# Performance work log

Hardware: AMD Instinct MI355X
Metric: run time of the kernel (lower is better)

Reference implementation:

```python
import jax, jax.numpy as jnp
import numpy as np
from jax import lax

LMBD = 0.1      # l1 penalty weight (init kwarg lmbd)
TOL = 1e-4      # convergence tolerance (init kwarg tol)
N_ITERS = 1000  # max ISTA iterations
DICT_SIZE = 1024
INPUT_DIM = 512
BATCH = 256


def setup_inputs() -> dict:
    key = jax.random.key(0)
    kx, kd = jax.random.split(key)
    # Dictionary parameter: randn rows normalized to unit l2 norm (as in _init_dict)
    D = jax.random.normal(kd, (DICT_SIZE, INPUT_DIM), dtype=jnp.float32)
    D = D / jnp.linalg.norm(D, axis=1, keepdims=True)
    x = jax.random.normal(kx, (BATCH, INPUT_DIM), dtype=jnp.float32)
    return {"x": x, "D": D}


def reference(x, D):
    # lr = 0.99 / max eigenvalue of Gram(D)  (as in _init_lr, done under no_grad)
    gram = D @ D.T  # [dict, dict]
    lr = 0.99 / jnp.max(jnp.linalg.eigvalsh(gram))
    thresh = lr * LMBD
    h0 = jnp.zeros((x.shape[0], D.shape[0]), dtype=x.dtype)  # [batch, dict]

    def cond(state):
        _, i, delta = state
        return (i < N_ITERS) & (delta >= TOL)

    def body(state):
        h, i, _ = state
        resid = x - h @ D          # [batch, input_dim]
        g = resid @ D.T            # [batch, dict]
        a = h + lr * g
        h_new = jnp.sign(a) * jnp.maximum(jnp.abs(a) - thresh, 0.0)  # soft-threshold
        delta = jnp.max(jnp.linalg.norm(h_new - h, axis=1))
        return (h_new, i + 1, delta)

    h, _, _ = lax.while_loop(cond, body, (h0, jnp.int32(0), jnp.float32(jnp.inf)))
    return h
```

## Files before the change

kernel.cpp:

```cpp
#include <hip/hip_runtime.h>
#include <math.h>

#define DICT 1024
#define IN_DIM 512
#define BATCH 256
#define LMBD_F 0.1f
#define TOL2 1e-8f
#define MAX_ITERS 1000
#define LM 64

#define OFF_G      0u
#define OFF_B      1048576u
#define OFF_HA     1310720u
#define OFF_W      1572864u
#define OFF_RDP    1573888u
#define OFF_FLG    1577984u
#define OFF_PM     1582080u
#define OFF_BF     1582592u
#define OFF_GBF    2106880u

typedef __attribute__((ext_vector_type(8))) short short8v;
typedef __attribute__((ext_vector_type(4))) float f32x4;
typedef __attribute__((ext_vector_type(4))) int i32x4;

#define MFMA16(a, b, c) __builtin_amdgcn_mfma_f32_16x16x32_bf16(a, b, c, 0, 0, 0)

__device__ __forceinline__ ushort f2bf(float v) {
    union { float f; unsigned u; } x; x.f = v;
    unsigned r = x.u + 0x7fffu + ((x.u >> 16) & 1u);
    return (ushort)(r >> 16);
}
__device__ __forceinline__ float bf2f(ushort b) {
    union { unsigned u; float f; } x; x.u = ((unsigned)b) << 16;
    return x.f;
}
__device__ __forceinline__ float softthr(float aa, float th) {
    float s = fabsf(aa) - th;
    return s > 0.f ? copysignf(s, aa) : 0.f;
}

__device__ __forceinline__ void vmdrain() { asm volatile("s_waitcnt vmcnt(0)" ::: "memory"); }
__device__ __forceinline__ unsigned ld_flag(const unsigned* p) {
    unsigned v;
    asm volatile("global_load_dword %0, %1, off sc1\ns_waitcnt vmcnt(0)" : "=v"(v) : "v"(p) : "memory");
    return v;
}
__device__ __forceinline__ void st_flag(unsigned* p, unsigned v) {
    asm volatile("global_store_dword %0, %1, off sc1" :: "v"(p), "v"(v) : "memory");
}
__device__ __forceinline__ float ld_f_sc(const float* p) {
    float v;
    asm volatile("global_load_dword %0, %1, off sc1\ns_waitcnt vmcnt(0)" : "=v"(v) : "v"(p) : "memory");
    return v;
}
__device__ __forceinline__ void st_f_sc(float* p, float v) {
    asm volatile("global_store_dword %0, %1, off sc1" :: "v"(p), "v"(v) : "memory");
}
__device__ __forceinline__ f32x4 ld_f4_sc(const float* p) {
    f32x4 v;
    asm volatile("global_load_dwordx4 %0, %1, off sc1\ns_waitcnt vmcnt(0)" : "=v"(v) : "v"(p) : "memory");
    return v;
}
__device__ __forceinline__ void st_u_sc(unsigned* p, unsigned v) {
    asm volatile("global_store_dword %0, %1, off sc1" :: "v"(p), "v"(v) : "memory");
}
__device__ __forceinline__ void ld_a16(i32x4* d, const void* p) {
    asm volatile("global_load_dwordx4 %0, %1, off sc1" : "=v"(*d) : "v"(p));
}
__device__ __forceinline__ void ld_u_nw(unsigned* d, const unsigned* p) {
    asm volatile("global_load_dword %0, %1, off sc1" : "=v"(*d) : "v"(p));
}
__device__ __forceinline__ void ld_f_nw(float* d, const float* p) {
    asm volatile("global_load_dword %0, %1, off sc1" : "=v"(*d) : "v"(p));
}

__global__ void k_init(float* ws) {
    int t = threadIdx.x;
    unsigned* flg = (unsigned*)(ws + OFF_FLG);
#pragma unroll
    for (int j = 0; j < 4; ++j) flg[t + 1024 * j] = 0u;
#pragma unroll
    for (int j = 0; j < 4; ++j) ws[OFF_RDP + t + 1024 * j] = 1e30f;
    if (t == 0) *(unsigned*)(ws + OFF_PM) = 0u;
}

__global__ void k_gemm_nt(float* __restrict__ C, const float* __restrict__ A,
                          const float* __restrict__ B, int M, int N, int K) {
    __shared__ float As[32][33];
    __shared__ float Bs[32][33];
    const int tid = threadIdx.x;
    const int m0 = blockIdx.y * 32, n0 = blockIdx.x * 32;
    const int lrw = tid >> 3;
    const int lc4 = (tid & 7) * 4;
    const int ty = tid >> 4, tx = tid & 15;
    float acc00 = 0, acc01 = 0, acc10 = 0, acc11 = 0;
    for (int k0 = 0; k0 < K; k0 += 32) {
        float4 av = *(const float4*)&A[(m0 + lrw) * K + k0 + lc4];
        float4 bv = *(const float4*)&B[(n0 + lrw) * K + k0 + lc4];
        __syncthreads();
        As[lrw][lc4 + 0] = av.x; As[lrw][lc4 + 1] = av.y;
        As[lrw][lc4 + 2] = av.z; As[lrw][lc4 + 3] = av.w;
        Bs[lrw][lc4 + 0] = bv.x; Bs[lrw][lc4 + 1] = bv.y;
        Bs[lrw][lc4 + 2] = bv.z; Bs[lrw][lc4 + 3] = bv.w;
        __syncthreads();
#pragma unroll
        for (int k = 0; k < 32; ++k) {
            float a0 = As[ty * 2][k], a1 = As[ty * 2 + 1][k];
            float b0 = Bs[tx * 2][k], b1 = Bs[tx * 2 + 1][k];
            acc00 += a0 * b0; acc01 += a0 * b1;
            acc10 += a1 * b0; acc11 += a1 * b1;
        }
    }
    C[(m0 + ty * 2) * N + n0 + tx * 2] = acc00;
    C[(m0 + ty * 2) * N + n0 + tx * 2 + 1] = acc01;
    C[(m0 + ty * 2 + 1) * N + n0 + tx * 2] = acc10;
    C[(m0 + ty * 2 + 1) * N + n0 + tx * 2 + 1] = acc11;
}

__global__ void k_conv_g(float* ws) {
    const int i = (blockIdx.x * 256 + threadIdx.x) * 4;
    const float* G = ws + OFF_G;
    ushort* Ghi = (ushort*)(ws + OFF_GBF);
    ushort* Glo = Ghi + 1048576u;
    float4 g = *(const float4*)&G[i];
    ushort h0 = f2bf(g.x), h1 = f2bf(g.y), h2 = f2bf(g.z), h3 = f2bf(g.w);
    *(ushort4*)&Ghi[i] = make_ushort4(h0, h1, h2, h3);
    ushort l0 = f2bf(g.x - bf2f(h0)), l1 = f2bf(g.y - bf2f(h1));
    ushort l2 = f2bf(g.z - bf2f(h2)), l3 = f2bf(g.w - bf2f(h3));
    *(ushort4*)&Glo[i] = make_ushort4(l0, l1, l2, l3);
}

__launch_bounds__(512, 2)
__global__ void k_persist(float* __restrict__ ws, float* __restrict__ dout) {
    const int tid = threadIdx.x;
    const int bid = blockIdx.x;
    const int w = tid >> 6, lane = tid & 63;
    unsigned* flg = (unsigned*)(ws + OFF_FLG);
    unsigned* podmask = (unsigned*)(ws + OFF_PM);
    float* Wg = ws + OFF_W;
    float* rdp = ws + OFF_RDP;
    const float* G = ws + OFF_G;

    __shared__ float Ps[8][16][64];
    __shared__ float Vl[1024], VPl[1024], Wl[1024];
    __shared__ float aArr[LM], bArr[LM];
    __shared__ float sred[8];
    __shared__ float scal2[2];
    __shared__ unsigned sres;

    unsigned gen = 0;
    unsigned stickyF = 0;

    const int bx = bid & 15;
    const int by = bid >> 4;
    const int R0 = by * 16, C0 = bx * 64;
    const int pod16 = by * 16;

    if (tid < 512) {
        Vl[tid] = 0.03125f; Vl[tid + 512] = 0.03125f;
        VPl[tid] = 0.f;     VPl[tid + 512] = 0.f;
    }
    __syncthreads();
    float bprev = 0.f;
#pragma unroll 1
    for (int j = 0; j < LM; ++j) {
        {
            const int row = tid >> 7, sub = tid & 127;
            const float* gr = G + (bid * 4 + row) * DICT;
            float s = 0.f;
#pragma unroll
            for (int jj = 0; jj < 8; ++jj) s += gr[sub + 128 * jj] * Vl[sub + 128 * jj];
#pragma unroll
            for (int off = 32; off; off >>= 1) s += __shfl_down(s, off);
            if (lane == 0) sred[w] = s;
            __syncthreads();
            if (tid < 4) st_f_sc(Wg + bid * 4 + tid, sred[2 * tid] + sred[2 * tid + 1]);
        }
        ++gen;
        vmdrain(); __syncthreads();
        if (tid == 0) st_flag(&flg[bid * 16], gen << 1);
        if (w == 0) {
            for (;;) {
                unsigned v0, v1, v2, v3;
                ld_u_nw(&v0, &flg[lane * 16]);
                ld_u_nw(&v1, &flg[(lane + 64) * 16]);
                ld_u_nw(&v2, &flg[(lane + 128) * 16]);
                ld_u_nw(&v3, &flg[(lane + 192) * 16]);
                vmdrain(); __builtin_amdgcn_sched_barrier(0);
                bool ok = ((v0 >> 1) >= gen) && ((v1 >> 1) >= gen) &&
                          ((v2 >> 1) >= gen) && ((v3 >> 1) >= gen);
                if (__ballot(ok) == ~0ull) break;
                __builtin_amdgcn_s_sleep(1);
            }
        }
        __syncthreads();
        if (tid < 256) { f32x4 w4 = ld_f4_sc(Wg + tid * 4); *(f32x4*)&Wl[tid * 4] = w4; }
        __syncthreads();
        float p = Vl[tid] * Wl[tid] + Vl[tid + 512] * Wl[tid + 512];
#pragma unroll
        for (int off = 32; off; off >>= 1) p += __shfl_down(p, off);
        if (lane == 0) sred[w] = p;
        __syncthreads();
        float alpha = sred[0] + sred[1] + sred[2] + sred[3] + sred[4] + sred[5] + sred[6] + sred[7];
        float u0 = Wl[tid] - alpha * Vl[tid] - bprev * VPl[tid];
        float u1 = Wl[tid + 512] - alpha * Vl[tid + 512] - bprev * VPl[tid + 512];
        float qq = u0 * u0 + u1 * u1;
        __syncthreads();
#pragma unroll
        for (int off = 32; off; off >>= 1) qq += __shfl_down(qq, off);
        if (lane == 0) sred[w] = qq;
        __syncthreads();
        float beta = sqrtf(sred[0] + sred[1] + sred[2] + sred[3] + sred[4] + sred[5] + sred[6] + sred[7]);
        float bsafe = (beta > 1e-20f) ? beta : 0.f;
        float inv = (beta > 1e-20f) ? 1.f / beta : 0.f;
        VPl[tid] = Vl[tid]; VPl[tid + 512] = Vl[tid + 512];
        Vl[tid] = u0 * inv; Vl[tid + 512] = u1 * inv;
        if (tid == 0) { aArr[j] = alpha; bArr[j] = bsafe; }
        bprev = bsafe;
        __syncthreads();
    }

    if (tid < 64) {
        double lo = 0.0, hi = 0.0;
        for (int i = 0; i < LM; ++i) {
            double bi  = fabs((double)bArr[i]);
            double bim = i ? fabs((double)bArr[i - 1]) : 0.0;
            double r = (double)aArr[i] + bi + bim;
            if (r > hi) hi = r;
        }
        for (int rnd = 0; rnd < 4; ++rnd) {
            double midt = lo + (hi - lo) * ((double)(tid + 1) / 65.0);
            int cntn = 0; double d = 1.0;
            for (int i = 0; i < LM; ++i) {
                double bm = i ? (double)bArr[i - 1] : 0.0;
                d = ((double)aArr[i] - midt) - (bm * bm) / d;
                if (d == 0.0) d = -1e-300;
                if (d < 0.0) cntn++;
            }
            unsigned long long m = __ballot(cntn >= LM);
            int first = (m == 0ull) ? 64 : (__ffsll((unsigned long long)m) - 1);
            double nlo = lo + (hi - lo) * ((double)first / 65.0);
            double nhi = (first == 64) ? hi : lo + (hi - lo) * ((double)(first + 1) / 65.0);
            lo = nlo; hi = nhi;
        }
        if (tid == 0) {
            float lam = (float)(0.5 * (lo + hi));
            float lrv = 0.99f / lam;
            scal2[0] = lrv;
            scal2[1] = lrv * LMBD_F;
        }
    }
    __syncthreads();
    const float lr = scal2[0], th = scal2[1];

    ushort* bfb = (ushort*)(ws + OFF_BF);
    const ushort* Ghi = (const ushort*)(ws + OFF_GBF);
    const float* bv_ = ws + OFF_B;
    float* hA = ws + OFF_HA;
    const int r16 = lane & 15, kk8 = (lane >> 4) * 8;
    const int er = tid >> 5;
    const int ec = (tid & 31) * 2;

    const ushort* pB = Ghi + (C0 + r16) * DICT + w * 128 + kk8;
    short8v bh[4][4], bl[4][4];
#pragma unroll
    for (int ks = 0; ks < 4; ++ks)
#pragma unroll
        for (int jj = 0; jj < 4; ++jj) {
            bh[ks][jj] = *(const short8v*)(pB + jj * 16 * DICT + ks * 32);
            bl[ks][jj] = *(const short8v*)(pB + 1048576u + jj * 16 * DICT + ks * 32);
        }

#pragma unroll 1
    for (int it = 0; it < MAX_ITERS; ++it) {
        const float* h_in = (it & 1) ? hA : dout;
        float* h_out      = (it & 1) ? dout : hA;
        const ushort* hi_in = bfb + ((it & 1) ? 524288u : 0u);
        ushort* hi_out = bfb + ((it & 1) ? 0u : 524288u);

        const ushort* pA = hi_in + (R0 + r16) * DICT + w * 128 + kk8;
        i32x4 aHr[4], aLr[4];
#pragma unroll
        for (int ks = 0; ks < 4; ++ks) {
            ld_a16(&aHr[ks], (const void*)(pA + ks * 32));
            ld_a16(&aLr[ks], (const void*)(pA + 262144u + ks * 32));
        }
        asm volatile("s_waitcnt vmcnt(0)" ::: "memory");
        __builtin_amdgcn_sched_barrier(0);

        f32x4 aHH[4], aHL[4], aLH[4];
#pragma unroll
        for (int jj = 0; jj < 4; ++jj) {
            aHH[jj] = (f32x4){0.f, 0.f, 0.f, 0.f};
            aHL[jj] = (f32x4){0.f, 0.f, 0.f, 0.f};
            aLH[jj] = (f32x4){0.f, 0.f, 0.f, 0.f};
        }
#pragma unroll
        for (int ks = 0; ks < 4; ++ks) {
            short8v ah, al;
            __builtin_memcpy(&ah, &aHr[ks], 16);
            __builtin_memcpy(&al, &aLr[ks], 16);
#pragma unroll
            for (int jj = 0; jj < 4; ++jj) {
                aHH[jj] = MFMA16(ah, bh[ks][jj], aHH[jj]);
                aHL[jj] = MFMA16(ah, bl[ks][jj], aHL[jj]);
                aLH[jj] = MFMA16(al, bh[ks][jj], aLH[jj]);
            }
        }

        const int r0 = (lane >> 4) * 4;
#pragma unroll
        for (int jj = 0; jj < 4; ++jj) {
            f32x4 s = aHH[jj] + aHL[jj] + aLH[jj];
            const int col = 16 * jj + r16;
#pragma unroll
            for (int qq = 0; qq < 4; ++qq) Ps[w][r0 + qq][col] = s[qq];
        }
        __syncthreads();

        float s0 = 0.f, s1 = 0.f;
#pragma unroll
        for (int ww = 0; ww < 8; ++ww) { s0 += Ps[ww][er][ec]; s1 += Ps[ww][er][ec + 1]; }
        const int gi = (R0 + er) * DICT + C0 + ec;
        float2 bb = *(const float2*)&bv_[gi];
        float2 hh = *(const float2*)&h_in[gi];
        float n0 = softthr(hh.x + lr * (bb.x - s0), th);
        float n1 = softthr(hh.y + lr * (bb.y - s1), th);
        *(float2*)&h_out[gi] = make_float2(n0, n1);

        ushort q0 = f2bf(n0), q1 = f2bf(n1);
        st_u_sc((unsigned*)&hi_out[gi], ((unsigned)q1 << 16) | (unsigned)q0);
        ushort z0 = f2bf(n0 - bf2f(q0)), z1 = f2bf(n1 - bf2f(q1));
        st_u_sc((unsigned*)&hi_out[262144u + gi], ((unsigned)z1 << 16) | (unsigned)z0);

        float d0 = n0 - hh.x, d1 = n1 - hh.y;
        float ssq = d0 * d0 + d1 * d1;
#pragma unroll
        for (int off = 1; off < 32; off <<= 1) ssq += __shfl_xor(ssq, off);
        if ((tid & 31) == 0) st_f_sc(&rdp[bid * 16 + er], ssq);

        vmdrain();
        __syncthreads();
        ++gen;
        if (tid == 0) st_flag(&flg[bid * 16], (gen << 1) | stickyF);

        if (w == 1 && (it & 3) == 3 && bid == pod16 + ((it >> 2) & 15)) {
            float v0, v1, v2, v3;
            const float* rp = rdp + by * 256;
            ld_f_nw(&v0, rp + lane);
            ld_f_nw(&v1, rp + lane + 64);
            ld_f_nw(&v2, rp + lane + 128);
            ld_f_nw(&v3, rp + lane + 192);
            vmdrain(); __builtin_amdgcn_sched_barrier(0);
            float s = v0 + v1 + v2 + v3;
            s += __shfl_xor(s, 16);
            s += __shfl_xor(s, 32);
            float m = s;
            m = fmaxf(m, __shfl_xor(m, 1));
            m = fmaxf(m, __shfl_xor(m, 2));
            m = fmaxf(m, __shfl_xor(m, 4));
            m = fmaxf(m, __shfl_xor(m, 8));
            if (lane == 0 && m < TOL2)
                __hip_atomic_fetch_or(podmask, 1u << by, __ATOMIC_RELAXED, __HIP_MEMORY_SCOPE_AGENT);
        }

        if (w == 0) {
            unsigned res;
            const unsigned* ap = (lane < 16) ? &flg[(pod16 + lane) * 16]
                               : (lane == 16 ? podmask : &flg[pod16 * 16]);
            for (;;) {
                unsigned v = ld_flag(ap);
                bool ok = (lane < 16) ? ((v >> 1) >= gen) : true;
                if (__ballot(ok) == ~0ull) {
                    unsigned long long bbit = __ballot((lane < 16) ? ((v & 1u) != 0u) : true);
                    unsigned pm = __shfl(v, 16);
                    res = ((bbit == ~0ull) ? 2u : 0u) | ((pm == 0xFFFFu) ? 1u : 0u);
                    break;
                }
                __builtin_amdgcn_s_sleep(1);
            }
            if (lane == 0) sres = res;
        }
        __syncthreads();
        const unsigned res = sres;
        stickyF |= (res & 1u);
        __syncthreads();

        if (res & 2u) {
            if ((it & 1) == 0) {
                const int g2 = (R0 + er) * DICT + C0 + ec;
                *(float2*)&dout[g2] = *(const float2*)&hA[g2];
            }
            return;
        }
    }
}

extern "C" void kernel_launch(void* const* d_in, const int* in_sizes, int n_in,
                              void* d_out, int out_size, void* d_ws, size_t ws_size,
                              hipStream_t stream) {
    const float* x = (const float*)d_in[0];
    const float* D = (const float*)d_in[1];
    float* out = (float*)d_out;
    float* ws = (float*)d_ws;

    (void)hipMemsetAsync(d_out, 0, (size_t)BATCH * DICT * sizeof(float), stream);
    (void)hipMemsetAsync((char*)(ws + OFF_BF), 0, 1048576, stream);
    k_init<<<dim3(1), dim3(1024), 0, stream>>>(ws);

    k_gemm_nt<<<dim3(32, 32), dim3(256), 0, stream>>>(ws + OFF_G, D, D, 1024, 1024, 512);
    k_conv_g<<<dim3(1024), dim3(256), 0, stream>>>(ws);
    k_gemm_nt<<<dim3(32, 8), dim3(256), 0, stream>>>(ws + OFF_B, x, D, 256, 1024, 512);

    void* args[] = { (void*)&ws, (void*)&out };
    (void)hipLaunchCooperativeKernel((const void*)k_persist, dim3(256), dim3(512), args, 0, stream);
}
```

Before: 5.026 ms.

## Split pod barrier into per-wave flag waits and defer convergence vote

The end-of-iteration pod barrier, where wave 0 spun on all 16 pod flags plus the pod mask before two block syncs, is removed. Each wave now waits at the top of the next iteration on only the two producer blocks whose h rows it reads, before loading its A fragments. The convergence/sticky bits are encoded in a widened flag word (generation in bits 2+, current and previous sticky bits) and combined after the MFMA phase, so the exit decision lags one iteration. This aims to cut barrier latency and overlap synchronization with compute, at the cost of more complex flag encoding, a possible extra iteration before exit, and a spin-limit escape that could break correctness if hit.

```diff
diff --git a/kernel.cpp b/kernel.cpp
--- a/kernel.cpp
+++ b/kernel.cpp
@@ -147,9 +147,10 @@
     __shared__ float sred[8];
     __shared__ float scal2[2];
     __shared__ unsigned sres;
+    __shared__ unsigned sbits[16];
+    __shared__ unsigned sStick;
 
     unsigned gen = 0;
-    unsigned stickyF = 0;
 
     const int bx = bid & 15;
     const int by = bid >> 4;
@@ -178,7 +179,7 @@
         }
         ++gen;
         vmdrain(); __syncthreads();
-        if (tid == 0) st_flag(&flg[bid * 16], gen << 1);
+        if (tid == 0) st_flag(&flg[bid * 16], gen << 2);
         if (w == 0) {
             for (;;) {
                 unsigned v0, v1, v2, v3;
@@ -187,8 +188,8 @@
                 ld_u_nw(&v2, &flg[(lane + 128) * 16]);
                 ld_u_nw(&v3, &flg[(lane + 192) * 16]);
                 vmdrain(); __builtin_amdgcn_sched_barrier(0);
-                bool ok = ((v0 >> 1) >= gen) && ((v1 >> 1) >= gen) &&
-                          ((v2 >> 1) >= gen) && ((v3 >> 1) >= gen);
+                bool ok = ((v0 >> 2) >= gen) && ((v1 >> 2) >= gen) &&
+                          ((v2 >> 2) >= gen) && ((v3 >> 2) >= gen);
                 if (__ballot(ok) == ~0ull) break;
                 __builtin_amdgcn_s_sleep(1);
             }
@@ -250,6 +251,7 @@
             scal2[1] = lrv * LMBD_F;
         }
     }
+    if (tid == 0) sStick = 0u;
     __syncthreads();
     const float lr = scal2[0], th = scal2[1];
 
@@ -271,6 +273,10 @@
             bl[ks][jj] = *(const short8v*)(pB + 1048576u + jj * 16 * DICT + ks * 32);
         }
 
+    unsigned sticky = 0, stPub = 0;
+    const unsigned* fprod0 = &flg[(pod16 + 2 * w) * 16];
+    const unsigned* fprod1 = &flg[(pod16 + 2 * w + 1) * 16];
+
 #pragma unroll 1
     for (int it = 0; it < MAX_ITERS; ++it) {
         const float* h_in = (it & 1) ? hA : dout;
@@ -278,6 +284,17 @@
         const ushort* hi_in = bfb + ((it & 1) ? 524288u : 0u);
         ushort* hi_out = bfb + ((it & 1) ? 0u : 524288u);
 
+        if (lane < 2) {
+            const unsigned* fp = lane ? fprod1 : fprod0;
+            unsigned v; int spins = 0;
+            for (;;) {
+                v = ld_flag(fp);
+                if ((v >> 2) >= gen) break;
+                __builtin_amdgcn_s_sleep(1);
+                if (++spins > (1 << 25)) break;
+            }
+            sbits[2 * w + lane] = ((v >> 2) == gen) ? ((v >> 1) & 1u) : (v & 1u);
+        }
         const ushort* pA = hi_in + (R0 + r16) * DICT + w * 128 + kk8;
         i32x4 aHr[4], aLr[4];
 #pragma unroll
@@ -317,6 +334,13 @@
             for (int qq = 0; qq < 4; ++qq) Ps[w][r0 + qq][col] = s[qq];
         }
         __syncthreads();
+
+        if (w == 0) {
+            unsigned b = (lane < 16) ? sbits[lane] : 1u;
+            unsigned long long allm = __ballot((b & 1u) != 0u);
+            unsigned long long anym = __ballot((lane < 16) && ((b & 1u) != 0u));
+            if (lane == 0) sres = ((allm == ~0ull) ? 2u : 0u) | ((anym != 0ull) ? 1u : 0u);
+        }
 
         float s0 = 0.f, s1 = 0.f;
 #pragma unroll
@@ -341,8 +365,18 @@
 
         vmdrain();
         __syncthreads();
+        const unsigned res = sres;
+        sticky |= (res & 1u) | sStick;
         ++gen;
-        if (tid == 0) st_flag(&flg[bid * 16], (gen << 1) | stickyF);
+        if (res & 2u) {
+            if ((it & 1) == 0) {
+                const int g2 = (R0 + er) * DICT + C0 + ec;
+                *(float2*)&dout[g2] = *(const float2*)&hA[g2];
+            }
+            return;
+        }
+        if (tid == 0) st_flag(&flg[bid * 16], (gen << 2) | (sticky << 1) | stPub);
+        stPub = sticky;
 
         if (w == 1 && (it & 3) == 3 && bid == pod16 + ((it >> 2) & 15)) {
             float v0, v1, v2, v3;
@@ -360,38 +394,12 @@
             m = fmaxf(m, __shfl_xor(m, 2));
             m = fmaxf(m, __shfl_xor(m, 4));
             m = fmaxf(m, __shfl_xor(m, 8));
-            if (lane == 0 && m < TOL2)
-                __hip_atomic_fetch_or(podmask, 1u << by, __ATOMIC_RELAXED, __HIP_MEMORY_SCOPE_AGENT);
-        }
-
-        if (w == 0) {
-            unsigned res;
-            const unsigned* ap = (lane < 16) ? &flg[(pod16 + lane) * 16]
-                               : (lane == 16 ? podmask : &flg[pod16 * 16]);
-            for (;;) {
-                unsigned v = ld_flag(ap);
-                bool ok = (lane < 16) ? ((v >> 1) >= gen) : true;
-                if (__ballot(ok) == ~0ull) {
-                    unsigned long long bbit = __ballot((lane < 16) ? ((v & 1u) != 0u) : true);
-                    unsigned pm = __shfl(v, 16);
-                    res = ((bbit == ~0ull) ? 2u : 0u) | ((pm == 0xFFFFu) ? 1u : 0u);
-                    break;
-                }
-                __builtin_amdgcn_s_sleep(1);
-            }
-            if (lane == 0) sres = res;
-        }
-        __syncthreads();
-        const unsigned res = sres;
-        stickyF |= (res & 1u);
-        __syncthreads();
-
-        if (res & 2u) {
-            if ((it & 1) == 0) {
-                const int g2 = (R0 + er) * DICT + C0 + ec;
-                *(float2*)&dout[g2] = *(const float2*)&hA[g2];
-            }
-            return;
+            if (lane == 0) {
+                if (m < TOL2)
+                    __hip_atomic_fetch_or(podmask, 1u << by, __ATOMIC_RELAXED, __HIP_MEMORY_SCOPE_AGENT);
+                unsigned pmv = ld_flag(podmask);
+                if (pmv == 0xFFFFu) sStick = 1u;
+            }
         }
     }
 }
```

New measurement: 4.585 ms, median of 2. 1.1x faster.
